# Optimization experiments

Hardware: AMD Instinct MI355X
Metric: run time of the kernel (lower is better)

Reference implementation:

```python
import jax, jax.numpy as jnp
import numpy as np

KERNEL_D = 3          # cv2 d=3 -> radius 1, 3x3 neighborhood
SIGMA_SPACE = 50.0
SIGMA_COLOR = 2.0
POOL = 16             # downsample_factor


def _bilateral3(x):
    # x: [B, H, W] single-channel images. cv2 BORDER_DEFAULT == REFLECT_101 == jnp 'reflect'.
    B, H, W = x.shape
    xp = jnp.pad(x, ((0, 0), (1, 1), (1, 1)), mode='reflect')
    inv2sc = 1.0 / (2.0 * SIGMA_COLOR * SIGMA_COLOR)
    inv2ss = 1.0 / (2.0 * SIGMA_SPACE * SIGMA_SPACE)
    num = jnp.zeros_like(x)
    den = jnp.zeros_like(x)
    for dy in (-1, 0, 1):
        for dx in (-1, 0, 1):
            nb = xp[:, 1 + dy:H + 1 + dy, 1 + dx:W + 1 + dx]
            ws = np.exp(-(dy * dy + dx * dx) * (1.0 / (2.0 * 50.0 * 50.0))).astype(np.float32)
            w = jnp.exp(-(nb - x) ** 2 * inv2sc) * ws
            num = num + w * nb
            den = den + w
    return num / den


def setup_inputs() -> dict:
    key = jax.random.key(0)
    x = jax.random.normal(key, (16, 1, 1024, 1024), dtype=jnp.float32)
    return {"x": x}


def reference(x):
    B, C, H, W = x.shape  # C == 1
    y = _bilateral3(x[:, 0])                       # [B, H, W]
    y = y[:, None]                                 # [B, 1, H, W]
    # AvgPool2d(16): non-overlapping 16x16 mean
    y = y.reshape(B, 1, H // POOL, POOL, W // POOL, POOL).mean(axis=(3, 5))
    return y
```

## Files before the change

kernel.cpp:

```cpp
#include <hip/hip_runtime.h>

#define IMG_H 1024
#define IMG_W 1024

#define CC  (-0.1803368801111244f)
#define WS1 (-2.8853900817779270e-4f)
#define WS2 (-5.7707801635558540e-4f)

__device__ __forceinline__ float edgew(float u, float v, float ws) {
    float d = u - v;
    return __builtin_amdgcn_exp2f(fmaf(d * d, CC, ws));
}

__global__ __launch_bounds__(512) void EdgePreserve_kernel(const float* __restrict__ x,
                                                           float* __restrict__ out) {
    const int t    = threadIdx.x;
    const int half = t >> 8;
    const int tt   = t & 255;

    const int bid = blockIdx.x;
    const int b   = bid >> 6;
    const int pr  = bid & 63;
    const int r0  = (pr << 4) + (half << 3);
    const int c0  = tt << 2;

    const float* base = x + (size_t)b * (IMG_H * IMG_W);
    const int cl = (c0 == 0) ? 1 : c0 - 1;
    const int cr = (c0 + 4 >= IMG_W) ? IMG_W - 2 : c0 + 4;

    float a0,a1,a2,a3,a4,a5, b0,b1,b2,b3,b4,b5, k0,k1,k2,k3,k4,k5, p0,p1,p2,p3,p4,p5;

#define LOADROW(q, d0,d1,d2,d3,d4,d5) { \
    int _r = r0 + (q); \
    int _rr = (_r < 0) ? -_r : ((_r >= IMG_H) ? (2*IMG_H-2-_r) : _r); \
    const float* _rp = base + _rr * IMG_W; \
    float4 _v = *reinterpret_cast<const float4*>(_rp + c0); \
    d0 = _rp[cl]; d1 = _v.x; d2 = _v.y; d3 = _v.z; d4 = _v.w; d5 = _rp[cr]; }

    LOADROW(-1, a0,a1,a2,a3,a4,a5)
    LOADROW( 0, b0,b1,b2,b3,b4,b5)
    LOADROW( 1, k0,k1,k2,k3,k4,k5)
    LOADROW( 2, p0,p1,p2,p3,p4,p5)

    float pV1 = edgew(a1,b1,WS1), pV2 = edgew(a2,b2,WS1), pV3 = edgew(a3,b3,WS1), pV4 = edgew(a4,b4,WS1);
    float pDL2 = edgew(a2,b1,WS2), pDL3 = edgew(a3,b2,WS2), pDL4 = edgew(a4,b3,WS2), pDL5 = edgew(a5,b4,WS2);
    float pDR0 = edgew(a0,b1,WS2), pDR1 = edgew(a1,b2,WS2), pDR2 = edgew(a2,b3,WS2), pDR3 = edgew(a3,b4,WS2);

    float psum = 0.0f;

    #pragma unroll
    for (int r = 0; r < 8; ++r) {
        float H0 = edgew(b0,b1,WS1), H1 = edgew(b1,b2,WS1), H2 = edgew(b2,b3,WS1),
              H3 = edgew(b3,b4,WS1), H4 = edgew(b4,b5,WS1);
        float V1  = edgew(b1,k1,WS1), V2  = edgew(b2,k2,WS1), V3  = edgew(b3,k3,WS1), V4 = edgew(b4,k4,WS1);
        float DL1 = edgew(b1,k0,WS2), DL2 = edgew(b2,k1,WS2), DL3 = edgew(b3,k2,WS2),
              DL4 = edgew(b4,k3,WS2), DL5 = edgew(b5,k4,WS2);
        float DR0 = edgew(b0,k1,WS2), DR1 = edgew(b1,k2,WS2), DR2 = edgew(b2,k3,WS2),
              DR3 = edgew(b3,k4,WS2), DR4 = edgew(b4,k5,WS2);

#define PIXEL(am,ac,ap, bm,bc,bp, km,kc,kp, wAL,wAC,wAR, wBL,wBR, wCL,wCV,wCR) { \
        float num = bc; \
        num = fmaf(wAL, am, num); num = fmaf(wAC, ac, num); num = fmaf(wAR, ap, num); \
        num = fmaf(wBL, bm, num); num = fmaf(wBR, bp, num); \
        num = fmaf(wCL, km, num); num = fmaf(wCV, kc, num); num = fmaf(wCR, kp, num); \
        float den = 1.0f + (((wAL + wAC) + (wAR + wBL)) + ((wBR + wCL) + (wCV + wCR))); \
        psum = fmaf(num, __builtin_amdgcn_rcpf(den), psum); }

        PIXEL(a0,a1,a2, b0,b1,b2, k0,k1,k2, pDR0,pV1,pDL2, H0,H1, DL1,V1,DR1)
        PIXEL(a1,a2,a3, b1,b2,b3, k1,k2,k3, pDR1,pV2,pDL3, H1,H2, DL2,V2,DR2)
        PIXEL(a2,a3,a4, b2,b3,b4, k2,k3,k4, pDR2,pV3,pDL4, H2,H3, DL3,V3,DR3)
        PIXEL(a3,a4,a5, b3,b4,b5, k3,k4,k5, pDR3,pV4,pDL5, H3,H4, DL4,V4,DR4)
#undef PIXEL

        a0=b0;a1=b1;a2=b2;a3=b3;a4=b4;a5=b5;
        b0=k0;b1=k1;b2=k2;b3=k3;b4=k4;b5=k5;
        k0=p0;k1=p1;k2=p2;k3=p3;k4=p4;k5=p5;
        pV1=V1;  pV2=V2;  pV3=V3;  pV4=V4;
        pDL2=DL2;pDL3=DL3;pDL4=DL4;pDL5=DL5;
        pDR0=DR0;pDR1=DR1;pDR2=DR2;pDR3=DR3;
        if (r < 6) { LOADROW(r+3, p0,p1,p2,p3,p4,p5) }
    }
#undef LOADROW

    psum += __shfl_xor(psum, 1);
    psum += __shfl_xor(psum, 2);

    __shared__ float red[64];
    if (half == 1 && (tt & 3) == 0) red[tt >> 2] = psum;
    __syncthreads();
    if (half == 0 && (tt & 3) == 0) {
        out[(size_t)bid * 64 + (tt >> 2)] = (psum + red[tt >> 2]) * (1.0f / 256.0f);
    }
}

extern "C" void kernel_launch(void* const* d_in, const int* in_sizes, int n_in,
                              void* d_out, int out_size, void* d_ws, size_t ws_size,
                              hipStream_t stream) {
    const float* x = (const float*)d_in[0];
    float* out     = (float*)d_out;
    EdgePreserve_kernel<<<dim3(16 * 64), dim3(512), 0, stream>>>(x, out);
}
```

Baseline: 27.18 us.

## Remap threads to 2-column by 16-row strips, drop shared-memory reduction

Each thread now processes 2 columns over all 16 rows of a pool tile instead of 4 columns over 8 rows. Blocks become 256 threads covering half an image row band, and the grid doubles. The pooled sum is reduced entirely with warp shuffles, which removes the shared-memory exchange and __syncthreads. The trade-off is more redundant edge-weight work and halo loads per output: each thread recomputes shared horizontal/diagonal weights at column boundaries, with a halo-to-interior ratio of 2:2 instead of 2:4, and the loads become float2 instead of float4.

```diff
diff --git a/kernel.cpp b/kernel.cpp
--- a/kernel.cpp
+++ b/kernel.cpp
@@ -12,51 +12,46 @@
     return __builtin_amdgcn_exp2f(fmaf(d * d, CC, ws));
 }
 
-__global__ __launch_bounds__(512) void EdgePreserve_kernel(const float* __restrict__ x,
+__global__ __launch_bounds__(256) void EdgePreserve_kernel(const float* __restrict__ x,
                                                            float* __restrict__ out) {
-    const int t    = threadIdx.x;
-    const int half = t >> 8;
-    const int tt   = t & 255;
-
+    const int t   = threadIdx.x;
     const int bid = blockIdx.x;
-    const int b   = bid >> 6;
-    const int pr  = bid & 63;
-    const int r0  = (pr << 4) + (half << 3);
-    const int c0  = tt << 2;
+    const int ch  = bid & 1;
+    const int pr  = (bid >> 1) & 63;
+    const int b   = bid >> 7;
+    const int r0  = pr << 4;
+    const int c0  = (ch << 9) + (t << 1);
 
     const float* base = x + (size_t)b * (IMG_H * IMG_W);
     const int cl = (c0 == 0) ? 1 : c0 - 1;
-    const int cr = (c0 + 4 >= IMG_W) ? IMG_W - 2 : c0 + 4;
+    const int cr = (c0 + 2 >= IMG_W) ? IMG_W - 2 : c0 + 2;
 
-    float a0,a1,a2,a3,a4,a5, b0,b1,b2,b3,b4,b5, k0,k1,k2,k3,k4,k5, p0,p1,p2,p3,p4,p5;
+    float a0,a1,a2,a3, b0,b1,b2,b3, k0,k1,k2,k3, p0,p1,p2,p3;
 
-#define LOADROW(q, d0,d1,d2,d3,d4,d5) { \
+#define LOADROW(q, d0,d1,d2,d3) { \
     int _r = r0 + (q); \
     int _rr = (_r < 0) ? -_r : ((_r >= IMG_H) ? (2*IMG_H-2-_r) : _r); \
     const float* _rp = base + _rr * IMG_W; \
-    float4 _v = *reinterpret_cast<const float4*>(_rp + c0); \
-    d0 = _rp[cl]; d1 = _v.x; d2 = _v.y; d3 = _v.z; d4 = _v.w; d5 = _rp[cr]; }
+    float2 _v = *reinterpret_cast<const float2*>(_rp + c0); \
+    d0 = _rp[cl]; d1 = _v.x; d2 = _v.y; d3 = _rp[cr]; }
 
-    LOADROW(-1, a0,a1,a2,a3,a4,a5)
-    LOADROW( 0, b0,b1,b2,b3,b4,b5)
-    LOADROW( 1, k0,k1,k2,k3,k4,k5)
-    LOADROW( 2, p0,p1,p2,p3,p4,p5)
+    LOADROW(-1, a0,a1,a2,a3)
+    LOADROW( 0, b0,b1,b2,b3)
+    LOADROW( 1, k0,k1,k2,k3)
+    LOADROW( 2, p0,p1,p2,p3)
 
-    float pV1 = edgew(a1,b1,WS1), pV2 = edgew(a2,b2,WS1), pV3 = edgew(a3,b3,WS1), pV4 = edgew(a4,b4,WS1);
-    float pDL2 = edgew(a2,b1,WS2), pDL3 = edgew(a3,b2,WS2), pDL4 = edgew(a4,b3,WS2), pDL5 = edgew(a5,b4,WS2);
-    float pDR0 = edgew(a0,b1,WS2), pDR1 = edgew(a1,b2,WS2), pDR2 = edgew(a2,b3,WS2), pDR3 = edgew(a3,b4,WS2);
+    float pV1  = edgew(a1,b1,WS1), pV2  = edgew(a2,b2,WS1);
+    float pDL2 = edgew(a2,b1,WS2), pDL3 = edgew(a3,b2,WS2);
+    float pDR0 = edgew(a0,b1,WS2), pDR1 = edgew(a1,b2,WS2);
 
     float psum = 0.0f;
 
     #pragma unroll
-    for (int r = 0; r < 8; ++r) {
-        float H0 = edgew(b0,b1,WS1), H1 = edgew(b1,b2,WS1), H2 = edgew(b2,b3,WS1),
-              H3 = edgew(b3,b4,WS1), H4 = edgew(b4,b5,WS1);
-        float V1  = edgew(b1,k1,WS1), V2  = edgew(b2,k2,WS1), V3  = edgew(b3,k3,WS1), V4 = edgew(b4,k4,WS1);
-        float DL1 = edgew(b1,k0,WS2), DL2 = edgew(b2,k1,WS2), DL3 = edgew(b3,k2,WS2),
-              DL4 = edgew(b4,k3,WS2), DL5 = edgew(b5,k4,WS2);
-        float DR0 = edgew(b0,k1,WS2), DR1 = edgew(b1,k2,WS2), DR2 = edgew(b2,k3,WS2),
-              DR3 = edgew(b3,k4,WS2), DR4 = edgew(b4,k5,WS2);
+    for (int r = 0; r < 16; ++r) {
+        float H0 = edgew(b0,b1,WS1), H1 = edgew(b1,b2,WS1), H2 = edgew(b2,b3,WS1);
+        float V1  = edgew(b1,k1,WS1), V2  = edgew(b2,k2,WS1);
+        float DL1 = edgew(b1,k0,WS2), DL2 = edgew(b2,k1,WS2), DL3 = edgew(b3,k2,WS2);
+        float DR0 = edgew(b0,k1,WS2), DR1 = edgew(b1,k2,WS2), DR2 = edgew(b2,k3,WS2);
 
 #define PIXEL(am,ac,ap, bm,bc,bp, km,kc,kp, wAL,wAC,wAR, wBL,wBR, wCL,wCV,wCR) { \
         float num = bc; \
@@ -68,28 +63,23 @@
 
         PIXEL(a0,a1,a2, b0,b1,b2, k0,k1,k2, pDR0,pV1,pDL2, H0,H1, DL1,V1,DR1)
         PIXEL(a1,a2,a3, b1,b2,b3, k1,k2,k3, pDR1,pV2,pDL3, H1,H2, DL2,V2,DR2)
-        PIXEL(a2,a3,a4, b2,b3,b4, k2,k3,k4, pDR2,pV3,pDL4, H2,H3, DL3,V3,DR3)
-        PIXEL(a3,a4,a5, b3,b4,b5, k3,k4,k5, pDR3,pV4,pDL5, H3,H4, DL4,V4,DR4)
 #undef PIXEL
 
-        a0=b0;a1=b1;a2=b2;a3=b3;a4=b4;a5=b5;
-        b0=k0;b1=k1;b2=k2;b3=k3;b4=k4;b5=k5;
-        k0=p0;k1=p1;k2=p2;k3=p3;k4=p4;k5=p5;
-        pV1=V1;  pV2=V2;  pV3=V3;  pV4=V4;
-        pDL2=DL2;pDL3=DL3;pDL4=DL4;pDL5=DL5;
-        pDR0=DR0;pDR1=DR1;pDR2=DR2;pDR3=DR3;
-        if (r < 6) { LOADROW(r+3, p0,p1,p2,p3,p4,p5) }
+        a0=b0;a1=b1;a2=b2;a3=b3;
+        b0=k0;b1=k1;b2=k2;b3=k3;
+        k0=p0;k1=p1;k2=p2;k3=p3;
+        pV1=V1; pV2=V2; pDL2=DL2; pDL3=DL3; pDR0=DR0; pDR1=DR1;
+        if (r < 14) { LOADROW(r+3, p0,p1,p2,p3) }
     }
 #undef LOADROW
 
     psum += __shfl_xor(psum, 1);
     psum += __shfl_xor(psum, 2);
+    psum += __shfl_xor(psum, 4);
 
-    __shared__ float red[64];
-    if (half == 1 && (tt & 3) == 0) red[tt >> 2] = psum;
-    __syncthreads();
-    if (half == 0 && (tt & 3) == 0) {
-        out[(size_t)bid * 64 + (tt >> 2)] = (psum + red[tt >> 2]) * (1.0f / 256.0f);
+    if ((t & 7) == 0) {
+        const int pc = (ch << 5) + (t >> 3);
+        out[(size_t)((b << 6) + pr) * 64 + pc] = psum * (1.0f / 256.0f);
     }
 }
 
@@ -98,5 +88,5 @@
                               hipStream_t stream) {
     const float* x = (const float*)d_in[0];
     float* out     = (float*)d_out;
-    EdgePreserve_kernel<<<dim3(16 * 64), dim3(512), 0, stream>>>(x, out);
+    EdgePreserve_kernel<<<dim3(16 * 64 * 2), dim3(256), 0, stream>>>(x, out);
 }
```

After: 28.22 us. 1.04x slower.
